# Kernel optimization log

Hardware: AMD Instinct MI355X
Metric: run time of the kernel (lower is better)

Reference implementation:

```python
import jax, jax.numpy as jnp
import numpy as np

N, E, EDGES, G = 4096, 256, 131072, 64
H, DH = 4, 64  # MHA heads, head dim


def _ln(x, g, b, eps=1e-5):
    m = jnp.mean(x, -1, keepdims=True)
    v = jnp.var(x, -1, keepdims=True)
    return g * (x - m) * jax.lax.rsqrt(v + eps) + b


def setup_inputs() -> dict:
    key = jax.random.key(0)
    ks = jax.random.split(key, 40)
    i = iter(range(40))
    def rn(shape, s=1.0):
        return jax.random.normal(ks[next(i)], shape, jnp.float32) * s
    w = lambda shape: rn(shape, 0.02)
    inp = {
        "node_hidden": rn((N, E)),
        "edge_hidden": rn((EDGES, E)),
        "pos": rn((N, 3)),
        # GINEConv MLP: Lin(E,2E) -> LN -> ReLU -> Dropout -> Lin(2E,E)
        "gine_w1": w((E, 2 * E)), "gine_b1": jnp.zeros((2 * E,)),
        "gine_ln_g": jnp.ones((2 * E,)), "gine_ln_b": jnp.zeros((2 * E,)),
        "gine_w2": w((2 * E, E)), "gine_b2": jnp.zeros((E,)),
        "norm1_g": jnp.ones((E,)), "norm1_b": jnp.zeros((E,)),
        # DirectionalMessagePassing params
        "dir_w": w((3, E)), "dir_b": jnp.zeros((E,)),
        "msg_w": w((E, E)), "msg_b": jnp.zeros((E,)),
        # MultiheadAttention
        "wq": w((E, E)), "bq": jnp.zeros((E,)),
        "wk": w((E, E)), "bk": jnp.zeros((E,)),
        "wv": w((E, E)), "bv": jnp.zeros((E,)),
        "wo": w((E, E)), "bo": jnp.zeros((E,)),
        # gate
        "gate_w": w((2 * E, E)), "gate_b": jnp.zeros((E,)),
        "norm2_g": jnp.ones((E,)), "norm2_b": jnp.zeros((E,)),
        # GraphNorm affine
        "gn_g": jnp.ones((E,)), "gn_b": jnp.zeros((E,)),
        # int inputs
        "edge_index": jax.random.randint(ks[next(i)], (2, EDGES), 0, N, jnp.int64 if jax.config.jax_enable_x64 else jnp.int32),
        "node_id": jnp.sort(jax.random.randint(ks[next(i)], (N,), 0, G)),
        "edge_id": jax.random.randint(ks[next(i)], (EDGES,), 0, G),
    }
    return inp


def reference(node_hidden, edge_hidden, pos,
              gine_w1, gine_b1, gine_ln_g, gine_ln_b, gine_w2, gine_b2,
              norm1_g, norm1_b, dir_w, dir_b, msg_w, msg_b,
              wq, bq, wk, bk, wv, bv, wo, bo,
              gate_w, gate_b, norm2_g, norm2_b, gn_g, gn_b,
              edge_index, node_id, edge_id):
    src, dst = edge_index[0], edge_index[1]
    identity = node_hidden

    # --- GINEConv: out = MLP(x + sum_j relu(x_j + e_ij)), eps=0 ---
    msg = jax.nn.relu(node_hidden[src] + edge_hidden)           # [EDGES, E]
    agg = jax.ops.segment_sum(msg, dst, num_segments=N)         # [N, E]
    h = node_hidden + agg
    h = jax.nn.relu(_ln(h @ gine_w1 + gine_b1, gine_ln_g, gine_ln_b))
    gnn_out = _ln(h @ gine_w2 + gine_b2, norm1_g, norm1_b)      # norm1

    # --- DirectionalMessagePassing over unit edge directions ---
    vec = pos[dst] - pos[src]                                   # [EDGES, 3]
    vec = vec / (jnp.linalg.norm(vec, axis=-1, keepdims=True) + 1e-8)
    dfeat = vec @ dir_w + dir_b                                 # [EDGES, E]
    smsg = gnn_out[src] * dfeat
    sagg = jax.ops.segment_sum(smsg, dst, num_segments=N)
    spatial_out = sagg @ msg_w + msg_b                          # [N, E]

    # --- MHA: q = gnn_out, k = v = spatial_out (seq = nodes, batch=1) ---
    q = (gnn_out @ wq + bq).reshape(N, H, DH)
    k = (spatial_out @ wk + bk).reshape(N, H, DH)
    v = (spatial_out @ wv + bv).reshape(N, H, DH)
    scores = jnp.einsum("nhd,mhd->hnm", q, k) / np.sqrt(DH)
    attn = jax.nn.softmax(scores, axis=-1)
    fused = jnp.einsum("hnm,mhd->nhd", attn, v).reshape(N, E) @ wo + bo

    # --- gated residual blend + norm2 ---
    gate = jax.nn.sigmoid(jnp.concatenate([fused, identity], -1) @ gate_w + gate_b)
    out = gate * fused + (1.0 - gate) * identity
    out = _ln(out, norm2_g, norm2_b)

    # --- GraphNorm: per-graph mean/var over nodes (segment stats) ---
    counts = jax.ops.segment_sum(jnp.ones((N, 1), out.dtype), node_id, num_segments=G)
    mean = jax.ops.segment_sum(out, node_id, num_segments=G) / counts
    cen = out - mean[node_id]
    var = jax.ops.segment_sum(cen * cen, node_id, num_segments=G) / counts
    out = gn_g * cen * jax.lax.rsqrt(var[node_id] + 1e-5) + gn_b

    # last_act = True; dropout is eval-mode identity
    return jax.nn.relu(out)
```

## Files before the change

### kernel.cpp

```cpp
#include <hip/hip_runtime.h>
#include <hip/hip_bf16.h>

#define N_NODES 4096
#define E_DIM   256
#define N_EDGES 131072
#define N_GRAPHS 64
#define H_HEADS 4
#define DH      64
#define SPLIT   4

typedef unsigned short u16;
typedef __attribute__((ext_vector_type(8))) short bf16x8;
typedef __attribute__((ext_vector_type(4))) float f32x4;

__device__ __forceinline__ float u2f(u16 u) {
    union { unsigned int i; float f; } c; c.i = ((unsigned int)u) << 16; return c.f;
}
__device__ __forceinline__ u16 f2bu(float f) {
    __hip_bfloat16 h = __float2bfloat16(f);
    return *reinterpret_cast<u16*>(&h);
}
__device__ __forceinline__ float ldv(const void* p, size_t i, int f32) {
    return f32 ? ((const float*)p)[i] : u2f(((const u16*)p)[i]);
}
__device__ __forceinline__ float4 ldv4(const void* p, size_t i, int f32) {
    if (f32) return *(const float4*)((const float*)p + i);
    ushort4 u = *(const ushort4*)((const u16*)p + i);
    return make_float4(u2f(u.x), u2f(u.y), u2f(u.z), u2f(u.w));
}
__device__ __forceinline__ float4 ldb4(const u16* p, size_t i) {
    ushort4 u = *(const ushort4*)(p + i);
    return make_float4(u2f(u.x), u2f(u.y), u2f(u.z), u2f(u.w));
}
__device__ __forceinline__ int chk_f32(const void* ones_raw) { return ((const u16*)ones_raw)[0] == 0; }
__device__ __forceinline__ int chk_i64(const int* ei) {
    return (ei[1] == 0 && ei[3] == 0 && ei[5] == 0 && ei[7] == 0);
}
__device__ __forceinline__ int ldi(const int* p, int i, int i64) {
    return i64 ? p[2 * i] : p[i];
}

struct SmDesc { const void* src; float* dst; int n; };
struct SmTable { SmDesc d[18]; };
struct WtDesc { const void* src; u16* dst; int K; int N; int base; };
struct WtTable { WtDesc d[8]; };

__global__ __launch_bounds__(256) void k_prep(const void* __restrict__ x_r, float* __restrict__ xf,
                                              u16* __restrict__ xh, const void* __restrict__ pos_r,
                                              float4* __restrict__ pos4, SmTable st, WtTable wt,
                                              const void* __restrict__ msgw_r, u16* __restrict__ msgwb,
                                              const void* __restrict__ wo_r, u16* __restrict__ wob,
                                              int* __restrict__ count, const void* __restrict__ ones_raw) {
    __shared__ u16 tile[64][68];
    int b = blockIdx.x, t = threadIdx.x;
    int f32 = chk_f32(ones_raw);
    if (b < 4096) {
        int i = b * 256 + t;
        float v = ldv(x_r, i, f32);
        xf[i] = v; xh[i] = f2bu(v);
        return;
    }
    b -= 4096;
    if (b < 16) {
        int n = b * 256 + t;
        pos4[n] = make_float4(ldv(pos_r, n * 3 + 0, f32), ldv(pos_r, n * 3 + 1, f32),
                              ldv(pos_r, n * 3 + 2, f32), 0.f);
        return;
    }
    b -= 16;
    if (b < 18 * 48) {
        int ti = b / 48;
        int off = (b % 48) * 256 + t;
        SmDesc e = st.d[ti];
        if (off < e.n) e.dst[off] = ldv(e.src, off, f32);
        return;
    }
    b -= 18 * 48;
    if (b < 160) {
        int i = 0;
        while (i < 7 && b >= wt.d[i + 1].base) i++;
        WtDesc e = wt.d[i];
        int tl = b - e.base;
        int ntn = e.N >> 6;
        int kt = tl / ntn, nt = tl % ntn;
        int r = t >> 2, c0 = (t & 3) * 16;
#pragma unroll
        for (int j = 0; j < 16; j++)
            tile[r][c0 + j] = f2bu(ldv(e.src, (size_t)(kt * 64 + r) * e.N + nt * 64 + c0 + j, f32));
        __syncthreads();
#pragma unroll
        for (int j = 0; j < 16; j++)
            e.dst[(size_t)(nt * 64 + r) * e.K + kt * 64 + c0 + j] = tile[c0 + j][r];
        return;
    }
    b -= 160;
    if (b < 256) { int i = b * 256 + t; msgwb[i] = f2bu(ldv(msgw_r, i, f32)); return; }
    b -= 256;
    if (b < 256) { int i = b * 256 + t; wob[i] = f2bu(ldv(wo_r, i, f32)); return; }
    b -= 256;
    count[b * 256 + t] = 0;
}

__global__ __launch_bounds__(256) void k_post(const u16* __restrict__ wot, const u16* __restrict__ foldT,
                                              const u16* __restrict__ gwt, u16* __restrict__ BT2,
                                              const float* __restrict__ bqf, const float* __restrict__ bkf,
                                              const float* __restrict__ bvf, const float* __restrict__ msgbf,
                                              const u16* __restrict__ wkvt, const float* __restrict__ bof,
                                              const float* __restrict__ gbf,
                                              float* __restrict__ bqkv, float* __restrict__ bias2) {
    int b = blockIdx.x, t = threadIdx.x;
    if (b < 1024) {
        int idx = b * 256 + t;
        int col = idx >> 9, k = idx & 511;
        u16 v;
        if (col < 256) v = (k < 256) ? wot[col * 256 + k] : (u16)0;
        else { int c = col - 256; v = (k < 256) ? foldT[c * 256 + k] : gwt[(size_t)c * 512 + k]; }
        BT2[idx] = v;
        return;
    }
    b -= 1024;
    if (b < 3) {
        int i = b * 256 + t;
        if (i < 256) { bqkv[i] = bqf[i]; return; }
        int c = i - 256;
        float s = (c < 256) ? bkf[c] : bvf[c - 256];
        const u16* row = wkvt + (size_t)c * 256;
        float acc = 0.f;
        for (int k = 0; k < 256; k++) acc = fmaf(msgbf[k], u2f(row[k]), acc);
        bqkv[256 + c] = s + acc;
    } else if (b == 3) {
        bias2[t] = bof[t];
    } else {
        float acc = gbf[t];
        const u16* row = gwt + (size_t)t * 512;
        for (int j = 0; j < 256; j++) acc = fmaf(bof[j], u2f(row[j]), acc);
        bias2[256 + t] = acc;
    }
}

__global__ __launch_bounds__(256) void k_mgemm(const void* __restrict__ A0, const void* __restrict__ A1,
                                               int as0, int as1, int abf0, int abf1,
                                               int K0, int Ktot, const u16* __restrict__ BT,
                                               const float* __restrict__ bias, void* __restrict__ C,
                                               int Nc, int outbf, int mode, u16* __restrict__ vt) {
    __shared__ u16 As[64 * 64];
    __shared__ u16 Bs[64 * 64];
    int t = threadIdx.x;
    int wv = t >> 6, l = t & 63, lg = l >> 4, lc = l & 15;
    int wm = wv >> 1, wn = wv & 1;
    int m0 = blockIdx.y * 64, n0 = blockIdx.x * 64;
    f32x4 acc[2][2] = {};
    int sr = t >> 2, sc = (t & 3) * 16;
    int sw = (sr & 7) << 3;

    for (int k0 = 0; k0 < Ktot; k0 += 64) {
        const void* Ab; int astr, kof, abf;
        if (mode == 1) { int pick = (n0 < K0); Ab = pick ? A0 : A1; astr = pick ? as0 : as1; abf = pick ? abf0 : abf1; kof = k0; }
        else if (k0 < K0) { Ab = A0; astr = as0; abf = abf0; kof = k0; }
        else { Ab = A1; astr = as1; abf = abf1; kof = k0 - K0; }
        if (abf) {
            const u16* Ap = (const u16*)Ab + (size_t)(m0 + sr) * astr + kof + sc;
            *(bf16x8*)&As[(sr * 64 + sc) ^ sw]     = *(const bf16x8*)Ap;
            *(bf16x8*)&As[(sr * 64 + sc + 8) ^ sw] = *(const bf16x8*)(Ap + 8);
        } else {
            const float* Ap = (const float*)Ab + (size_t)(m0 + sr) * astr + kof + sc;
#pragma unroll
            for (int j = 0; j < 2; j++) {
                float4 f0 = *(const float4*)(Ap + j * 8);
                float4 f1 = *(const float4*)(Ap + j * 8 + 4);
                bf16x8 bv;
                bv[0] = (short)f2bu(f0.x); bv[1] = (short)f2bu(f0.y);
                bv[2] = (short)f2bu(f0.z); bv[3] = (short)f2bu(f0.w);
                bv[4] = (short)f2bu(f1.x); bv[5] = (short)f2bu(f1.y);
                bv[6] = (short)f2bu(f1.z); bv[7] = (short)f2bu(f1.w);
                *(bf16x8*)&As[(sr * 64 + sc + j * 8) ^ sw] = bv;
            }
        }
        const u16* Bp = BT + (size_t)(n0 + sr) * Ktot + k0 + sc;
        *(bf16x8*)&Bs[(sr * 64 + sc) ^ sw]     = *(const bf16x8*)Bp;
        *(bf16x8*)&Bs[(sr * 64 + sc + 8) ^ sw] = *(const bf16x8*)(Bp + 8);
        __syncthreads();
#pragma unroll
        for (int ks = 0; ks < 2; ks++) {
            bf16x8 af[2], bfr[2];
#pragma unroll
            for (int mi = 0; mi < 2; mi++) {
                int row = wm * 32 + mi * 16 + lc;
                af[mi] = *(const bf16x8*)&As[(row * 64 + ks * 32 + lg * 8) ^ ((row & 7) << 3)];
            }
#pragma unroll
            for (int ni = 0; ni < 2; ni++) {
                int col = wn * 32 + ni * 16 + lc;
                bfr[ni] = *(const bf16x8*)&Bs[(col * 64 + ks * 32 + lg * 8) ^ ((col & 7) << 3)];
            }
#pragma unroll
            for (int mi = 0; mi < 2; mi++)
#pragma unroll
                for (int ni = 0; ni < 2; ni++)
                    acc[mi][ni] = __builtin_amdgcn_mfma_f32_16x16x32_bf16(af[mi], bfr[ni], acc[mi][ni], 0, 0, 0);
        }
        __syncthreads();
    }
#pragma unroll
    for (int mi = 0; mi < 2; mi++)
#pragma unroll
        for (int ni = 0; ni < 2; ni++) {
            int col = n0 + wn * 32 + ni * 16 + lc;
            float bb = bias ? bias[col] : 0.f;
#pragma unroll
            for (int r = 0; r < 4; r++) {
                int row = m0 + wm * 32 + mi * 16 + lg * 4 + r;
                float v = acc[mi][ni][r] + bb;
                u16 hb = f2bu(v);
                if (outbf) ((u16*)C)[(size_t)row * Nc + col] = hb;
                else       ((float*)C)[(size_t)row * Nc + col] = v;
                if (vt && col >= 512) vt[(size_t)(col - 512) * N_NODES + row] = hb;
            }
        }
}

__global__ __launch_bounds__(256) void k_attn(const u16* __restrict__ QKV, const u16* __restrict__ VT,
                                              u16* __restrict__ part) {
    __shared__ u16 K_lds[64 * 64];
    __shared__ u16 V_lds[64 * 64];
    int t = threadIdx.x;
    int wv = t >> 6, l = t & 63;
    int lg = l >> 4, lc = l & 15;
    int h = blockIdx.y, c = blockIdx.z;
    int q0 = blockIdx.x * 64 + wv * 16;
    const float SC = 0.18033688f;

    bf16x8 qf[2];
#pragma unroll
    for (int kk = 0; kk < 2; kk++)
        qf[kk] = *(const bf16x8*)&QKV[(size_t)(q0 + lc) * 768 + h * DH + kk * 32 + lg * 8];

    f32x4 oacc[4] = {};
    float mx = -1e30f, lsum = 0.f;

    int lr = t >> 2, lc16 = (t & 3) * 16;
    int src_a = ((lg & 1) * 2) * 16 + lc;
    int src_b = src_a + 16;

    for (int kv0 = c * (N_NODES / SPLIT); kv0 < (c + 1) * (N_NODES / SPLIT); kv0 += 64) {
        __syncthreads();
        {
            int base = lr * 64 + lc16;
            int sw = (lr & 7) << 3;
            const u16* kp = &QKV[(size_t)(kv0 + lr) * 768 + 256 + h * DH + lc16];
            *(bf16x8*)&K_lds[(base) ^ sw]     = *(const bf16x8*)kp;
            *(bf16x8*)&K_lds[(base + 8) ^ sw] = *(const bf16x8*)(kp + 8);
            const u16* vp = &VT[((size_t)h * DH + lr) * N_NODES + kv0 + lc16];
            *(bf16x8*)&V_lds[(base) ^ sw]     = *(const bf16x8*)vp;
            *(bf16x8*)&V_lds[(base + 8) ^ sw] = *(const bf16x8*)(vp + 8);
        }
        __syncthreads();

        f32x4 s[4];
#pragma unroll
        for (int n = 0; n < 4; n++) {
            f32x4 a = {};
#pragma unroll
            for (int kk = 0; kk < 2; kk++) {
                int row = n * 16 + lc;
                bf16x8 kf = *(const bf16x8*)&K_lds[(row * 64 + kk * 32 + lg * 8) ^ ((row & 7) << 3)];
                a = __builtin_amdgcn_mfma_f32_16x16x32_bf16(kf, qf[kk], a, 0, 0, 0);
            }
            s[n] = a;
        }
        float tm = -1e30f;
#pragma unroll
        for (int n = 0; n < 4; n++)
#pragma unroll
            for (int r = 0; r < 4; r++) { s[n][r] *= SC; tm = fmaxf(tm, s[n][r]); }
        tm = fmaxf(tm, __shfl_xor(tm, 16));
        tm = fmaxf(tm, __shfl_xor(tm, 32));
        float nm = fmaxf(mx, tm);
        float alpha = exp2f(mx - nm);
        mx = nm;
        float p[4][4], ps = 0.f;
#pragma unroll
        for (int n = 0; n < 4; n++)
#pragma unroll
            for (int r = 0; r < 4; r++) { p[n][r] = exp2f(s[n][r] - nm); ps += p[n][r]; }
        ps += __shfl_xor(ps, 16);
        ps += __shfl_xor(ps, 32);
        lsum = lsum * alpha + ps;

        float af[4];
#pragma unroll
        for (int r = 0; r < 4; r++) af[r] = __shfl(alpha, lg * 4 + r);
#pragma unroll
        for (int n = 0; n < 4; n++)
#pragma unroll
            for (int r = 0; r < 4; r++) oacc[n][r] *= af[r];

        unsigned int pk[8];
#pragma unroll
        for (int n = 0; n < 4; n++) {
            pk[n * 2 + 0] = (unsigned int)f2bu(p[n][0]) | ((unsigned int)f2bu(p[n][1]) << 16);
            pk[n * 2 + 1] = (unsigned int)f2bu(p[n][2]) | ((unsigned int)f2bu(p[n][3]) << 16);
        }
#pragma unroll
        for (int kc = 0; kc < 2; kc++) {
            int n1 = kc * 2 + (lg >> 1);
            union { unsigned int w[4]; bf16x8 v; } u;
            u.w[0] = __shfl(pk[n1 * 2 + 0], src_a);
            u.w[1] = __shfl(pk[n1 * 2 + 1], src_a);
            u.w[2] = __shfl(pk[n1 * 2 + 0], src_b);
            u.w[3] = __shfl(pk[n1 * 2 + 1], src_b);
#pragma unroll
            for (int n = 0; n < 4; n++) {
                int row = n * 16 + lc;
                bf16x8 b = *(const bf16x8*)&V_lds[(row * 64 + kc * 32 + lg * 8) ^ ((row & 7) << 3)];
                oacc[n] = __builtin_amdgcn_mfma_f32_16x16x32_bf16(u.v, b, oacc[n], 0, 0, 0);
            }
        }
    }

    float lf[4], mf[4];
#pragma unroll
    for (int r = 0; r < 4; r++) {
        lf[r] = __shfl(lsum, lg * 4 + r);
        mf[r] = __shfl(mx, lg * 4 + r);
    }
#pragma unroll
    for (int r = 0; r < 4; r++) {
        u16* pp = part + ((size_t)(c * H_HEADS + h) * N_NODES + q0 + lg * 4 + r) * 72;
#pragma unroll
        for (int n = 0; n < 4; n++) pp[n * 16 + lc] = f2bu(oacc[n][r]);
        if (lc == 0) { *(float*)(pp + 64) = mf[r]; *(float*)(pp + 66) = lf[r]; }
    }
}

__global__ __launch_bounds__(256) void k_combine(const u16* __restrict__ part, u16* __restrict__ attnoh) {
    int n = blockIdx.x, t = threadIdx.x;
    int h = t >> 6, d = t & 63;
    float M = -1e30f;
#pragma unroll
    for (int c = 0; c < SPLIT; c++)
        M = fmaxf(M, *(const float*)(part + ((size_t)(c * H_HEADS + h) * N_NODES + n) * 72 + 64));
    float L = 0.f, o = 0.f;
#pragma unroll
    for (int c = 0; c < SPLIT; c++) {
        const u16* pp = part + ((size_t)(c * H_HEADS + h) * N_NODES + n) * 72;
        float w = exp2f(*(const float*)(pp + 64) - M);
        L = fmaf(*(const float*)(pp + 66), w, L);
        o = fmaf(u2f(pp[d]), w, o);
    }
    attnoh[(size_t)n * E_DIM + h * DH + d] = f2bu(o / L);
}

__device__ __forceinline__ void block_red2(float& a, float& b, float* sbuf) {
#pragma unroll
    for (int o = 32; o > 0; o >>= 1) { a += __shfl_down(a, o); b += __shfl_down(b, o); }
    int w = threadIdx.x >> 6;
    if ((threadIdx.x & 63) == 0) { sbuf[w] = a; sbuf[4 + w] = b; }
    __syncthreads();
    a = sbuf[0] + sbuf[1] + sbuf[2] + sbuf[3];
    b = sbuf[4] + sbuf[5] + sbuf[6] + sbuf[7];
    __syncthreads();
}

__global__ void k_count(const int* __restrict__ ei, int* __restrict__ count) {
    int e = blockIdx.x * 256 + threadIdx.x;
    int i64 = chk_i64(ei);
    int d = i64 ? ei[2 * (N_EDGES + e)] : ei[N_EDGES + e];
    atomicAdd(&count[d], 1);
}

__global__ __launch_bounds__(1024) void k_scan(const int* __restrict__ count,
                                               int* __restrict__ offs, int* __restrict__ cursor) {
    __shared__ int wsum[16];
    int t = threadIdx.x, lane = t & 63, wid = t >> 6;
    int c0 = count[t * 4 + 0], c1 = count[t * 4 + 1], c2 = count[t * 4 + 2], c3 = count[t * 4 + 3];
    int tot = c0 + c1 + c2 + c3;
    int inc = tot;
#pragma unroll
    for (int o = 1; o < 64; o <<= 1) { int v = __shfl_up(inc, o); if (lane >= o) inc += v; }
    if (lane == 63) wsum[wid] = inc;
    __syncthreads();
    if (t < 16) {
        int v = wsum[t];
#pragma unroll
        for (int o = 1; o < 16; o <<= 1) { int u = __shfl_up(v, o); if (t >= o) v += u; }
        wsum[t] = v;
    }
    __syncthreads();
    int base = (wid ? wsum[wid - 1] : 0) + inc - tot;
    int o0 = base, o1 = base + c0, o2 = o1 + c1, o3 = o2 + c2;
    offs[t * 4 + 0] = o0; offs[t * 4 + 1] = o1; offs[t * 4 + 2] = o2; offs[t * 4 + 3] = o3;
    cursor[t * 4 + 0] = o0; cursor[t * 4 + 1] = o1; cursor[t * 4 + 2] = o2; cursor[t * 4 + 3] = o3;
    if (t == 1023) offs[4096] = wsum[15];
}

__global__ void k_scatter(const int* __restrict__ ei, int* __restrict__ cursor,
                          int2* __restrict__ elist2) {
    int e = blockIdx.x * 256 + threadIdx.x;
    int i64 = chk_i64(ei);
    int s = i64 ? ei[2 * e] : ei[e];
    int d = i64 ? ei[2 * (N_EDGES + e)] : ei[N_EDGES + e];
    int p = atomicAdd(&cursor[d], 1);
    elist2[p] = make_int2(e, s);
}

__global__ __launch_bounds__(256) void k_gine_agg(const float* __restrict__ xf, const u16* __restrict__ xh,
                                                  const void* __restrict__ eh, const void* __restrict__ ones_raw,
                                                  const int* __restrict__ offs, const int2* __restrict__ elist2,
                                                  u16* __restrict__ houth) {
    int wv = threadIdx.x >> 6, ld = threadIdx.x & 63;
    int n = blockIdx.x * 4 + wv;
    int f32 = chk_f32(ones_raw);
    int cc = ld * 4;
    float4 acc = *(const float4*)&xf[(size_t)n * E_DIM + cc];
    int i0 = offs[n], i1 = offs[n + 1];
    int i = i0;
    for (; i + 4 <= i1; i += 4) {
        int2 es[4];
#pragma unroll
        for (int j = 0; j < 4; j++) es[j] = elist2[i + j];
        float4 a[4], x[4];
#pragma unroll
        for (int j = 0; j < 4; j++) a[j] = ldv4(eh, (size_t)es[j].x * E_DIM + cc, f32);
#pragma unroll
        for (int j = 0; j < 4; j++) x[j] = ldb4(xh, (size_t)es[j].y * E_DIM + cc);
#pragma unroll
        for (int j = 0; j < 4; j++) {
            acc.x += fmaxf(x[j].x + a[j].x, 0.f);
            acc.y += fmaxf(x[j].y + a[j].y, 0.f);
            acc.z += fmaxf(x[j].z + a[j].z, 0.f);
            acc.w += fmaxf(x[j].w + a[j].w, 0.f);
        }
    }
    for (; i < i1; i++) {
        int2 es = elist2[i];
        float4 a0 = ldv4(eh, (size_t)es.x * E_DIM + cc, f32);
        float4 x0 = ldb4(xh, (size_t)es.y * E_DIM + cc);
        acc.x += fmaxf(x0.x + a0.x, 0.f);
        acc.y += fmaxf(x0.y + a0.y, 0.f);
        acc.z += fmaxf(x0.z + a0.z, 0.f);
        acc.w += fmaxf(x0.w + a0.w, 0.f);
    }
    ushort4 o;
    o.x = f2bu(acc.x); o.y = f2bu(acc.y); o.z = f2bu(acc.z); o.w = f2bu(acc.w);
    *(ushort4*)&houth[(size_t)n * E_DIM + cc] = o;
}

template <int W, int OUTBF>
__global__ __launch_bounds__(256) void k_ln(const float* __restrict__ in, void* __restrict__ out,
                                            const float* __restrict__ g, const float* __restrict__ b,
                                            int relu) {
    __shared__ float sbuf[8];
    constexpr int PE = W / 256;
    int n = blockIdx.x, t = threadIdx.x;
    const float* row = in + (size_t)n * W;
    float x[PE];
    float s = 0.f, s2 = 0.f;
#pragma unroll
    for (int i = 0; i < PE; i++) { x[i] = row[t + i * 256]; s += x[i]; s2 += x[i] * x[i]; }
    block_red2(s, s2, sbuf);
    float mean = s / W;
    float var = fmaxf(s2 / W - mean * mean, 0.f);
    float rstd = rsqrtf(var + 1e-5f);
#pragma unroll
    for (int i = 0; i < PE; i++) {
        int c = t + i * 256;
        float y = g[c] * (x[i] - mean) * rstd + b[c];
        if (relu) y = fmaxf(y, 0.f);
        if (OUTBF) ((u16*)out)[(size_t)n * W + c] = f2bu(y);
        else       ((float*)out)[(size_t)n * W + c] = y;
    }
}

__global__ __launch_bounds__(256) void k_dir(const float4* __restrict__ pos4, const int* __restrict__ offs,
                                             const int2* __restrict__ elist2, const u16* __restrict__ gnnh,
                                             const float* __restrict__ dw, const float* __restrict__ db,
                                             u16* __restrict__ saggh) {
    int wv = threadIdx.x >> 6, ld = threadIdx.x & 63;
    int n = blockIdx.x * 4 + wv;
    int cc = ld * 4;
    float4 w0 = *(const float4*)&dw[cc];
    float4 w1 = *(const float4*)&dw[256 + cc];
    float4 w2 = *(const float4*)&dw[512 + cc];
    float4 bb = *(const float4*)&db[cc];
    float4 pn = pos4[n];
    float4 acc = {0.f, 0.f, 0.f, 0.f};
    int i0 = offs[n], i1 = offs[n + 1];
    int i = i0;
    for (; i + 2 <= i1; i += 2) {
        int2 es0 = elist2[i], es1 = elist2[i + 1];
        float4 p0 = pos4[es0.y], p1 = pos4[es1.y];
        float4 g0 = ldb4(gnnh, (size_t)es0.y * E_DIM + cc);
        float4 g1 = ldb4(gnnh, (size_t)es1.y * E_DIM + cc);
        float vx0 = pn.x - p0.x, vy0 = pn.y - p0.y, vz0 = pn.z - p0.z;
        float vx1 = pn.x - p1.x, vy1 = pn.y - p1.y, vz1 = pn.z - p1.z;
        float rn0 = 1.f / (sqrtf(vx0 * vx0 + vy0 * vy0 + vz0 * vz0) + 1e-8f);
        float rn1 = 1.f / (sqrtf(vx1 * vx1 + vy1 * vy1 + vz1 * vz1) + 1e-8f);
        acc.x = fmaf(g0.x, bb.x + (vx0 * w0.x + vy0 * w1.x + vz0 * w2.x) * rn0, acc.x);
        acc.y = fmaf(g0.y, bb.y + (vx0 * w0.y + vy0 * w1.y + vz0 * w2.y) * rn0, acc.y);
        acc.z = fmaf(g0.z, bb.z + (vx0 * w0.z + vy0 * w1.z + vz0 * w2.z) * rn0, acc.z);
        acc.w = fmaf(g0.w, bb.w + (vx0 * w0.w + vy0 * w1.w + vz0 * w2.w) * rn0, acc.w);
        acc.x = fmaf(g1.x, bb.x + (vx1 * w0.x + vy1 * w1.x + vz1 * w2.x) * rn1, acc.x);
        acc.y = fmaf(g1.y, bb.y + (vx1 * w0.y + vy1 * w1.y + vz1 * w2.y) * rn1, acc.y);
        acc.z = fmaf(g1.z, bb.z + (vx1 * w0.z + vy1 * w1.z + vz1 * w2.z) * rn1, acc.z);
        acc.w = fmaf(g1.w, bb.w + (vx1 * w0.w + vy1 * w1.w + vz1 * w2.w) * rn1, acc.w);
    }
    if (i < i1) {
        int2 es0 = elist2[i];
        float4 p0 = pos4[es0.y];
        float4 g0 = ldb4(gnnh, (size_t)es0.y * E_DIM + cc);
        float vx0 = pn.x - p0.x, vy0 = pn.y - p0.y, vz0 = pn.z - p0.z;
        float rn0 = 1.f / (sqrtf(vx0 * vx0 + vy0 * vy0 + vz0 * vz0) + 1e-8f);
        acc.x = fmaf(g0.x, bb.x + (vx0 * w0.x + vy0 * w1.x + vz0 * w2.x) * rn0, acc.x);
        acc.y = fmaf(g0.y, bb.y + (vx0 * w0.y + vy0 * w1.y + vz0 * w2.y) * rn0, acc.y);
        acc.z = fmaf(g0.z, bb.z + (vx0 * w0.z + vy0 * w1.z + vz0 * w2.z) * rn0, acc.z);
        acc.w = fmaf(g0.w, bb.w + (vx0 * w0.w + vy0 * w1.w + vz0 * w2.w) * rn0, acc.w);
    }
    ushort4 o;
    o.x = f2bu(acc.x); o.y = f2bu(acc.y); o.z = f2bu(acc.z); o.w = f2bu(acc.w);
    *(ushort4*)&saggh[(size_t)n * E_DIM + cc] = o;
}

__global__ __launch_bounds__(256) void k_gate_ln(const float* __restrict__ fg, const float* __restrict__ xf,
                                                 const float* __restrict__ g2, const float* __restrict__ b2,
                                                 float* __restrict__ out2) {
    __shared__ float sbuf[8];
    int n = blockIdx.x, t = threadIdx.x;
    float fu = fg[(size_t)n * 512 + t];
    float z  = fg[(size_t)n * 512 + 256 + t];
    float gate = 1.f / (1.f + __expf(-z));
    float o = gate * fu + (1.f - gate) * xf[(size_t)n * E_DIM + t];
    float s = o, s2 = o * o;
    block_red2(s, s2, sbuf);
    float mean = s / E_DIM;
    float var = fmaxf(s2 / E_DIM - mean * mean, 0.f);
    float y = g2[t] * (o - mean) * rsqrtf(var + 1e-5f) + b2[t];
    out2[(size_t)n * E_DIM + t] = y;
}

__device__ __forceinline__ int lbound(const int* __restrict__ nid, int v, int i64) {
    int lo = 0, hi = N_NODES;
    while (lo < hi) { int mid = (lo + hi) >> 1; if (ldi(nid, mid, i64) < v) lo = mid + 1; else hi = mid; }
    return lo;
}

__global__ __launch_bounds__(256) void k_gnstats(const int* __restrict__ nid, const int* __restrict__ ei,
                                                 const float* __restrict__ out2, float* __restrict__ gnp) {
    int g = blockIdx.x >> 3, ch = blockIdx.x & 7, t = threadIdx.x;
    int i64 = chk_i64(ei);
    int a = lbound(nid, g, i64), b = lbound(nid, g + 1, i64);
    int len = b - a;
    int s0 = a + (len * ch) / 8, s1 = a + (len * (ch + 1)) / 8;
    float s = 0.f, s2 = 0.f;
    for (int n = s0; n < s1; n++) {
        float x = out2[(size_t)n * E_DIM + t];
        s += x; s2 = fmaf(x, x, s2);
    }
    gnp[((size_t)(g * 8 + ch) * 2 + 0) * 256 + t] = s;
    gnp[((size_t)(g * 8 + ch) * 2 + 1) * 256 + t] = s2;
}

__global__ __launch_bounds__(256) void k_gnapply(const float* __restrict__ out2, const int* __restrict__ nid,
                                                 const int* __restrict__ ei, const void* __restrict__ ones_raw,
                                                 const float* __restrict__ gnp,
                                                 const float* __restrict__ gg, const float* __restrict__ gb,
                                                 void* __restrict__ out) {
    int n = blockIdx.x, t = threadIdx.x;
    int i64 = chk_i64(ei);
    int g = ldi(nid, n, i64);
    int a = lbound(nid, g, i64), b = lbound(nid, g + 1, i64);
    float inv = 1.f / (float)(b - a);
    float s = 0.f, s2 = 0.f;
#pragma unroll
    for (int ch = 0; ch < 8; ch++) {
        s  += gnp[((size_t)(g * 8 + ch) * 2 + 0) * 256 + t];
        s2 += gnp[((size_t)(g * 8 + ch) * 2 + 1) * 256 + t];
    }
    float mean = s * inv;
    float var = fmaxf(s2 * inv - mean * mean, 0.f);
    float y = gg[t] * (out2[(size_t)n * E_DIM + t] - mean) * rsqrtf(var + 1e-5f) + gb[t];
    y = fmaxf(y, 0.f);
    size_t idx = (size_t)n * E_DIM + t;
    if (chk_f32(ones_raw)) ((float*)out)[idx] = y;
    else ((__hip_bfloat16*)out)[idx] = __float2bfloat16(y);
}

extern "C" void kernel_launch(void* const* d_in, const int* in_sizes, int n_in,
                              void* d_out, int out_size, void* d_ws, size_t ws_size,
                              hipStream_t stream) {
    const void* x_r    = d_in[0];
    const void* eh_r   = d_in[1];
    const void* pos_r  = d_in[2];
    const void* w1_r   = d_in[3];
    const void* b1_r   = d_in[4];
    const void* glng_r = d_in[5];
    const void* glnb_r = d_in[6];
    const void* w2_r   = d_in[7];
    const void* b2_r   = d_in[8];
    const void* n1g_r  = d_in[9];
    const void* n1b_r  = d_in[10];
    const void* dirw_r = d_in[11];
    const void* dirb_r = d_in[12];
    const void* msgw_r = d_in[13];
    const void* msgb_r = d_in[14];
    const void* wq_r   = d_in[15];
    const void* bq_r   = d_in[16];
    const void* wk_r   = d_in[17];
    const void* bk_r   = d_in[18];
    const void* wv_r   = d_in[19];
    const void* bv_r   = d_in[20];
    const void* wo_r   = d_in[21];
    const void* bo_r   = d_in[22];
    const void* gw_r   = d_in[23];
    const void* gb_r   = d_in[24];
    const void* n2g_r  = d_in[25];
    const void* n2b_r  = d_in[26];
    const void* gng_r  = d_in[27];
    const void* gnb_r  = d_in[28];
    const int* ei      = (const int*)d_in[29];
    const int* nid     = (const int*)d_in[30];

    char* ws = (char*)d_ws;
    const size_t KB = 1 << 10, MB = 1 << 20;
    int*   count  = (int*)(ws + 0);
    int*   offs   = (int*)(ws + 32 * KB);
    int*   cursor = (int*)(ws + 64 * KB);
    int2*  elist2 = (int2*)(ws + 128 * KB);

    float* prm    = (float*)(ws + 1 * MB + 192 * KB);
    float* b1f   = prm + 0;
    float* glngf = prm + 512,  *glnbf = prm + 1024;
    float* b2f   = prm + 1536;
    float* n1gf  = prm + 1792, *n1bf  = prm + 2048;
    float* dirwf = prm + 2304;
    float* dirbf = prm + 3072, *msgbf = prm + 3328;
    float* bqf   = prm + 3584, *bkf   = prm + 3840, *bvf = prm + 4096, *bof = prm + 4352;
    float* gbf   = prm + 4608;
    float* n2gf  = prm + 4864, *n2bf  = prm + 5120;
    float* gngf  = prm + 5376, *gnbf  = prm + 5632;
    float4* pos4 = (float4*)(ws + 1 * MB + 256 * KB);

    u16* w1t    = (u16*)(ws + 2 * MB);
    u16* w2t    = (u16*)(ws + 2 * MB + 256 * KB);
    u16* wot    = (u16*)(ws + 2 * MB + 512 * KB);
    u16* gwt    = (u16*)(ws + 2 * MB + 640 * KB);
    u16* wqkvt  = (u16*)(ws + 3 * MB);
    u16* wkvt   = (u16*)(ws + 3 * MB + 384 * KB);
    u16* msgwb  = (u16*)(ws + 3 * MB + 640 * KB);
    u16* wob    = (u16*)(ws + 3 * MB + 768 * KB);
    u16* foldT  = (u16*)(ws + 3 * MB + 896 * KB);
    u16* BT2    = (u16*)(ws + 4 * MB);
    float* bias2f = (float*)(ws + 4 * MB + 512 * KB);
    float* bqkvf  = (float*)(ws + 4 * MB + 516 * KB);

    float* xf     = (float*)(ws + 5 * MB);
    u16*   xh     = (u16*)(ws + 9 * MB);
    u16*   hbufh  = (u16*)(ws + 11 * MB);
    float* T1     = (float*)(ws + 13 * MB);
    float* gnnf   = (float*)(ws + 21 * MB);
    u16*   gnnh   = (u16*)(ws + 25 * MB);
    u16*   saggh  = (u16*)(ws + 27 * MB);
    u16*   QKVh   = (u16*)(ws + 29 * MB);
    u16*   VT     = (u16*)(ws + 35 * MB);
    u16*   part   = (u16*)(ws + 37 * MB);
    u16*   attnoh = (u16*)(ws + 11 * MB);
    float* fg     = (float*)(ws + 13 * MB);
    float* out2   = (float*)(ws + 21 * MB);
    float* gnp    = (float*)(ws + 25 * MB);

    SmTable st;
    {
        int i = 0;
        auto add = [&](const void* s, float* d, int n) { st.d[i].src = s; st.d[i].dst = d; st.d[i].n = n; i++; };
        add(b1_r, b1f, 512); add(glng_r, glngf, 512); add(glnb_r, glnbf, 512);
        add(b2_r, b2f, 256); add(n1g_r, n1gf, 256); add(n1b_r, n1bf, 256);
        add(dirw_r, dirwf, 768); add(dirb_r, dirbf, 256); add(msgb_r, msgbf, 256);
        add(bq_r, bqf, 256); add(bk_r, bkf, 256); add(bv_r, bvf, 256); add(bo_r, bof, 256);
        add(gb_r, gbf, 256); add(n2g_r, n2gf, 256); add(n2b_r, n2bf, 256);
        add(gng_r, gngf, 256); add(gnb_r, gnbf, 256);
    }
    WtTable wt;
    {
        int i = 0, base = 0;
        auto add = [&](const void* s, u16* d, int K, int N) {
            wt.d[i].src = s; wt.d[i].dst = d; wt.d[i].K = K; wt.d[i].N = N; wt.d[i].base = base;
            base += (K / 64) * (N / 64); i++;
        };
        add(w1_r, w1t, 256, 512);
        add(w2_r, w2t, 512, 256);
        add(wq_r, wqkvt, 256, 256);
        add(wk_r, wkvt, 256, 256);
        add(wv_r, wkvt + 256 * 256, 256, 256);
        add(wo_r, wot, 256, 256);
        add(gw_r, gwt, 512, 256);
        wt.d[7].base = 0x7fffffff;
    }
    k_prep<<<4096 + 16 + 18 * 48 + 160 + 256 + 256 + 16, 256, 0, stream>>>(
        x_r, xf, xh, pos_r, pos4, st, wt, msgw_r, msgwb, wo_r, wob, count, glng_r);

    k_count<<<N_EDGES / 256, 256, 0, stream>>>(ei, count);
    k_scan<<<1, 1024, 0, stream>>>(count, offs, cursor);
    k_scatter<<<N_EDGES / 256, 256, 0, stream>>>(ei, cursor, elist2);

    k_mgemm<<<dim3(4, 8), 256, 0, stream>>>(wkvt, nullptr, 256, 0, 1, 0, 256, 256, msgwb,
                                            nullptr, wqkvt + 256 * 256, 256, 1, 0, nullptr);
    k_mgemm<<<dim3(4, 4), 256, 0, stream>>>(gwt, nullptr, 512, 0, 1, 0, 256, 256, wob,
                                            nullptr, foldT, 256, 1, 0, nullptr);
    k_post<<<1029, 256, 0, stream>>>(wot, foldT, gwt, BT2, bqf, bkf, bvf, msgbf, wkvt,
                                     bof, gbf, bqkvf, bias2f);

    k_gine_agg<<<N_NODES / 4, 256, 0, stream>>>(xf, xh, eh_r, glng_r, offs, elist2, hbufh);
    k_mgemm<<<dim3(8, 64), 256, 0, stream>>>(hbufh, nullptr, 256, 0, 1, 0, 256, 256, w1t,
                                             b1f, T1, 512, 0, 0, nullptr);
    k_ln<512, 0><<<N_NODES, 256, 0, stream>>>(T1, T1, glngf, glnbf, 1);
    k_mgemm<<<dim3(4, 64), 256, 0, stream>>>(T1, nullptr, 512, 0, 0, 0, 512, 512, w2t,
                                             b2f, gnnf, 256, 0, 0, nullptr);
    k_ln<256, 1><<<N_NODES, 256, 0, stream>>>(gnnf, gnnh, n1gf, n1bf, 0);

    k_dir<<<N_NODES / 4, 256, 0, stream>>>(pos4, offs, elist2, gnnh, dirwf, dirbf, saggh);

    k_mgemm<<<dim3(12, 64), 256, 0, stream>>>(gnnh, saggh, 256, 256, 1, 1, 256, 256, wqkvt,
                                              bqkvf, QKVh, 768, 1, 1, VT);

    k_attn<<<dim3(N_NODES / 64, H_HEADS, SPLIT), 256, 0, stream>>>(QKVh, VT, part);
    k_combine<<<N_NODES, 256, 0, stream>>>(part, attnoh);

    k_mgemm<<<dim3(8, 64), 256, 0, stream>>>(attnoh, xf, 256, 256, 1, 0, 256, 512, BT2,
                                             bias2f, fg, 512, 0, 0, nullptr);
    k_gate_ln<<<N_NODES, 256, 0, stream>>>(fg, xf, n2gf, n2bf, out2);

    k_gnstats<<<N_GRAPHS * 8, 256, 0, stream>>>(nid, ei, out2, gnp);
    k_gnapply<<<N_NODES, 256, 0, stream>>>(out2, nid, ei, glng_r, gnp, gngf, gnbf, d_out);
}
```

Measured before the change: 241.3 us.

## Load attention K/V straight from global, use bf16 inputs for GEMMs

```diff
diff --git a/kernel.cpp b/kernel.cpp
--- a/kernel.cpp
+++ b/kernel.cpp
@@ -221,8 +221,6 @@
 
 __global__ __launch_bounds__(256) void k_attn(const u16* __restrict__ QKV, const u16* __restrict__ VT,
                                               u16* __restrict__ part) {
-    __shared__ u16 K_lds[64 * 64];
-    __shared__ u16 V_lds[64 * 64];
     int t = threadIdx.x;
     int wv = t >> 6, l = t & 63;
     int lg = l >> 4, lc = l & 15;
@@ -238,32 +236,19 @@
     f32x4 oacc[4] = {};
     float mx = -1e30f, lsum = 0.f;
 
-    int lr = t >> 2, lc16 = (t & 3) * 16;
     int src_a = ((lg & 1) * 2) * 16 + lc;
     int src_b = src_a + 16;
+    const u16* Kbase = QKV + 256 + h * DH + lg * 8;
+    const u16* Vbase = VT + (size_t)h * DH * N_NODES + lg * 8;
 
     for (int kv0 = c * (N_NODES / SPLIT); kv0 < (c + 1) * (N_NODES / SPLIT); kv0 += 64) {
-        __syncthreads();
-        {
-            int base = lr * 64 + lc16;
-            int sw = (lr & 7) << 3;
-            const u16* kp = &QKV[(size_t)(kv0 + lr) * 768 + 256 + h * DH + lc16];
-            *(bf16x8*)&K_lds[(base) ^ sw]     = *(const bf16x8*)kp;
-            *(bf16x8*)&K_lds[(base + 8) ^ sw] = *(const bf16x8*)(kp + 8);
-            const u16* vp = &VT[((size_t)h * DH + lr) * N_NODES + kv0 + lc16];
-            *(bf16x8*)&V_lds[(base) ^ sw]     = *(const bf16x8*)vp;
-            *(bf16x8*)&V_lds[(base + 8) ^ sw] = *(const bf16x8*)(vp + 8);
-        }
-        __syncthreads();
-
         f32x4 s[4];
 #pragma unroll
         for (int n = 0; n < 4; n++) {
             f32x4 a = {};
 #pragma unroll
             for (int kk = 0; kk < 2; kk++) {
-                int row = n * 16 + lc;
-                bf16x8 kf = *(const bf16x8*)&K_lds[(row * 64 + kk * 32 + lg * 8) ^ ((row & 7) << 3)];
+                bf16x8 kf = *(const bf16x8*)&Kbase[(size_t)(kv0 + n * 16 + lc) * 768 + kk * 32];
                 a = __builtin_amdgcn_mfma_f32_16x16x32_bf16(kf, qf[kk], a, 0, 0, 0);
             }
             s[n] = a;
@@ -311,9 +296,8 @@
             u.w[3] = __shfl(pk[n1 * 2 + 1], src_b);
 #pragma unroll
             for (int n = 0; n < 4; n++) {
-                int row = n * 16 + lc;
-                bf16x8 b = *(const bf16x8*)&V_lds[(row * 64 + kc * 32 + lg * 8) ^ ((row & 7) << 3)];
-                oacc[n] = __builtin_amdgcn_mfma_f32_16x16x32_bf16(u.v, b, oacc[n], 0, 0, 0);
+                bf16x8 vf = *(const bf16x8*)&Vbase[(size_t)(n * 16 + lc) * N_NODES + kv0 + kc * 32];
+                oacc[n] = __builtin_amdgcn_mfma_f32_16x16x32_bf16(u.v, vf, oacc[n], 0, 0, 0);
             }
         }
     }
@@ -663,6 +647,7 @@
     u16*   QKVh   = (u16*)(ws + 29 * MB);
     u16*   VT     = (u16*)(ws + 35 * MB);
     u16*   part   = (u16*)(ws + 37 * MB);
+    u16*   T1h    = (u16*)(ws + 47 * MB);
     u16*   attnoh = (u16*)(ws + 11 * MB);
     float* fg     = (float*)(ws + 13 * MB);
     float* out2   = (float*)(ws + 21 * MB);
@@ -712,8 +697,8 @@
     k_gine_agg<<<N_NODES / 4, 256, 0, stream>>>(xf, xh, eh_r, glng_r, offs, elist2, hbufh);
     k_mgemm<<<dim3(8, 64), 256, 0, stream>>>(hbufh, nullptr, 256, 0, 1, 0, 256, 256, w1t,
                                              b1f, T1, 512, 0, 0, nullptr);
-    k_ln<512, 0><<<N_NODES, 256, 0, stream>>>(T1, T1, glngf, glnbf, 1);
-    k_mgemm<<<dim3(4, 64), 256, 0, stream>>>(T1, nullptr, 512, 0, 0, 0, 512, 512, w2t,
+    k_ln<512, 1><<<N_NODES, 256, 0, stream>>>(T1, T1h, glngf, glnbf, 1);
+    k_mgemm<<<dim3(4, 64), 256, 0, stream>>>(T1h, nullptr, 512, 0, 1, 0, 512, 512, w2t,
                                              b2f, gnnf, 256, 0, 0, nullptr);
     k_ln<256, 1><<<N_NODES, 256, 0, stream>>>(gnnf, gnnh, n1gf, n1bf, 0);
 
@@ -725,7 +710,7 @@
     k_attn<<<dim3(N_NODES / 64, H_HEADS, SPLIT), 256, 0, stream>>>(QKVh, VT, part);
     k_combine<<<N_NODES, 256, 0, stream>>>(part, attnoh);
 
-    k_mgemm<<<dim3(8, 64), 256, 0, stream>>>(attnoh, xf, 256, 256, 1, 0, 256, 512, BT2,
+    k_mgemm<<<dim3(8, 64), 256, 0, stream>>>(attnoh, xh, 256, 256, 1, 1, 256, 512, BT2,
                                              bias2f, fg, 512, 0, 0, nullptr);
     k_gate_ln<<<N_NODES, 256, 0, stream>>>(fg, xf, n2gf, n2bf, out2);
 
```

Measured after the change: 305.1 us. 1.26x slower.
